# Performance work log

Hardware: AMD Instinct MI355X
Metric: run time of the kernel (lower is better)

Reference implementation:

```python
import jax, jax.numpy as jnp
import numpy as np

N_POINTS = 16384
N_SAMPLES = 8192


def setup_inputs() -> dict:
    key = jax.random.key(0)
    k1, k2, k3, k4 = jax.random.split(key, 4)
    a = jax.random.normal(k1, (3, N_POINTS), dtype=jnp.float32)
    b = jax.random.normal(k2, (3, N_POINTS), dtype=jnp.float32)
    # stand-ins for np.random.shuffle(...)[:n_samples] in the torch forward
    a_idx = jax.random.randint(k3, (N_SAMPLES,), 0, N_POINTS, dtype=jnp.int64)
    b_idx = jax.random.randint(k4, (N_SAMPLES,), 0, N_POINTS, dtype=jnp.int64)
    return {"a": a, "b": b, "a_idx": a_idx, "b_idx": b_idx}


def reference(a, b, a_idx, b_idx):
    # a, b: [3, N]; sample n_samples columns, transpose -> [n, 3], keep xyz
    pa = a[:, a_idx].T[:, :3]  # [n, 3]
    pb = b[:, b_idx].T[:, :3]  # [n, 3]
    # d[k, i] = ||pa_i - pb_k||^2, via ||a||^2 + ||b||^2 - 2 b.a^T
    # (avoids the original's [n, n, 3] broadcasted difference tensor)
    sq_a = jnp.sum(pa * pa, axis=1)  # [n]
    sq_b = jnp.sum(pb * pb, axis=1)  # [n]
    d = sq_a[None, :] + sq_b[:, None] - 2.0 * (pb @ pa.T)  # [n, n]
    # torch.min(d, 0)[0].sum(): min over b-points for each a-point, then sum
    return jnp.min(d, axis=0).sum()
```

## Files before the change

kernel.cpp:

```cpp
#include <hip/hip_runtime.h>
#include <stdint.h>


#define BLOCK   256
#define NPTS_A  8
#define BPTS    128

__device__ __forceinline__ unsigned enc_f32(float f) {
    unsigned u = __float_as_uint(f);
    return (u & 0x80000000u) ? ~u : (u | 0x80000000u);
}
__device__ __forceinline__ float dec_f32(unsigned u) {
    return (u & 0x80000000u) ? __uint_as_float(u & 0x7FFFFFFFu)
                             : __uint_as_float(~u);
}

__global__ __launch_bounds__(BLOCK)
void chamfer_min_kernel(const float* __restrict__ a,
                        const float* __restrict__ b,
                        const int* __restrict__ a_idx,
                        const int* __restrict__ b_idx,
                        unsigned* __restrict__ minarr,
                        int N, int a_chunks) {
    __shared__ float4 tile[BPTS];
    const int bid = blockIdx.x;
    const int ac  = bid % a_chunks;
    const int bc  = bid / a_chunks;
    const int tid = threadIdx.x;

    if (tid < BPTS) {
        int j  = bc * BPTS + tid;
        int bi = b_idx[j];
        float bx = b[bi], by = b[N + bi], bz = b[2 * N + bi];
        tile[tid] = make_float4(-2.f * bx, -2.f * by, -2.f * bz,
                                bx * bx + by * by + bz * bz);
    }
    __syncthreads();

    float ax[NPTS_A], ay[NPTS_A], az[NPTS_A], mn[NPTS_A];
    int   ii[NPTS_A];
#pragma unroll
    for (int m = 0; m < NPTS_A; ++m) {
        int i = ac * (BLOCK * NPTS_A) + m * BLOCK + tid;
        ii[m] = i;
        int ai = a_idx[i];
        ax[m] = a[ai]; ay[m] = a[N + ai]; az[m] = a[2 * N + ai];
        mn[m] = 3.4e38f;
    }

    for (int k = 0; k < BPTS; ++k) {
        float4 t = tile[k];
#pragma unroll
        for (int m = 0; m < NPTS_A; ++m) {
            float c = fmaf(t.x, ax[m], fmaf(t.y, ay[m], fmaf(t.z, az[m], t.w)));
            mn[m] = fminf(mn[m], c);
        }
    }

#pragma unroll
    for (int m = 0; m < NPTS_A; ++m)
        atomicMin(&minarr[ii[m]], enc_f32(mn[m]));
}

__global__ __launch_bounds__(BLOCK)
void chamfer_reduce_kernel(const float* __restrict__ a,
                           const int* __restrict__ a_idx,
                           const unsigned* __restrict__ minarr,
                           float* __restrict__ out, int N, int n) {
    int i = blockIdx.x * blockDim.x + threadIdx.x;
    float v = 0.f;
    if (i < n) {
        float f  = dec_f32(minarr[i]);
        int   ai = a_idx[i];
        float ax = a[ai], ay = a[N + ai], az = a[2 * N + ai];
        v = f + ax * ax + ay * ay + az * az;
    }
#pragma unroll
    for (int off = 32; off > 0; off >>= 1)
        v += __shfl_down(v, off, 64);
    if ((threadIdx.x & 63) == 0)
        atomicAdd(out, v);
}

extern "C" void kernel_launch(void* const* d_in, const int* in_sizes, int n_in,
                              void* d_out, int out_size, void* d_ws, size_t ws_size,
                              hipStream_t stream) {
    const float* a     = (const float*)d_in[0];
    const float* b     = (const float*)d_in[1];
    const int*   a_idx = (const int*)d_in[2];
    const int*   b_idx = (const int*)d_in[3];
    float*       out   = (float*)d_out;

    const int N = in_sizes[0] / 3;
    const int n = in_sizes[2];

    unsigned* minarr = (unsigned*)d_ws;

    hipMemsetAsync(minarr, 0xFF, (size_t)n * sizeof(unsigned), stream);
    hipMemsetAsync(out, 0, sizeof(float), stream);

    const int a_chunks = n / (BLOCK * NPTS_A);
    const int b_chunks = n / BPTS;
    chamfer_min_kernel<<<a_chunks * b_chunks, BLOCK, 0, stream>>>(
        a, b, a_idx, b_idx, minarr, N, a_chunks);

    chamfer_reduce_kernel<<<(n + BLOCK - 1) / BLOCK, BLOCK, 0, stream>>>(
        a, a_idx, minarr, out, N, n);
}
```

Baseline: 81.48 us.

## Replace atomicMin with per-chunk partial minima and deterministic two-stage reduction

```diff
diff --git a/kernel.cpp b/kernel.cpp
--- a/kernel.cpp
+++ b/kernel.cpp
@@ -4,24 +4,15 @@
 
 #define BLOCK   256
 #define NPTS_A  8
-#define BPTS    128
-
-__device__ __forceinline__ unsigned enc_f32(float f) {
-    unsigned u = __float_as_uint(f);
-    return (u & 0x80000000u) ? ~u : (u | 0x80000000u);
-}
-__device__ __forceinline__ float dec_f32(unsigned u) {
-    return (u & 0x80000000u) ? __uint_as_float(u & 0x7FFFFFFFu)
-                             : __uint_as_float(~u);
-}
+#define BPTS    64
 
 __global__ __launch_bounds__(BLOCK)
 void chamfer_min_kernel(const float* __restrict__ a,
                         const float* __restrict__ b,
                         const int* __restrict__ a_idx,
                         const int* __restrict__ b_idx,
-                        unsigned* __restrict__ minarr,
-                        int N, int a_chunks) {
+                        float* __restrict__ pmin,
+                        int N, int n, int a_chunks) {
     __shared__ float4 tile[BPTS];
     const int bid = blockIdx.x;
     const int ac  = bid % a_chunks;
@@ -38,16 +29,15 @@
     __syncthreads();
 
     float ax[NPTS_A], ay[NPTS_A], az[NPTS_A], mn[NPTS_A];
-    int   ii[NPTS_A];
 #pragma unroll
     for (int m = 0; m < NPTS_A; ++m) {
         int i = ac * (BLOCK * NPTS_A) + m * BLOCK + tid;
-        ii[m] = i;
         int ai = a_idx[i];
         ax[m] = a[ai]; ay[m] = a[N + ai]; az[m] = a[2 * N + ai];
         mn[m] = 3.4e38f;
     }
 
+#pragma unroll 4
     for (int k = 0; k < BPTS; ++k) {
         float4 t = tile[k];
 #pragma unroll
@@ -58,28 +48,52 @@
     }
 
 #pragma unroll
-    for (int m = 0; m < NPTS_A; ++m)
-        atomicMin(&minarr[ii[m]], enc_f32(mn[m]));
+    for (int m = 0; m < NPTS_A; ++m) {
+        int i = ac * (BLOCK * NPTS_A) + m * BLOCK + tid;
+        pmin[(size_t)bc * n + i] = mn[m];
+    }
 }
 
 __global__ __launch_bounds__(BLOCK)
-void chamfer_reduce_kernel(const float* __restrict__ a,
-                           const int* __restrict__ a_idx,
-                           const unsigned* __restrict__ minarr,
-                           float* __restrict__ out, int N, int n) {
-    int i = blockIdx.x * blockDim.x + threadIdx.x;
-    float v = 0.f;
-    if (i < n) {
-        float f  = dec_f32(minarr[i]);
-        int   ai = a_idx[i];
-        float ax = a[ai], ay = a[N + ai], az = a[2 * N + ai];
-        v = f + ax * ax + ay * ay + az * az;
-    }
+void chamfer_colmin_sum_kernel(const float* __restrict__ a,
+                               const int* __restrict__ a_idx,
+                               const float* __restrict__ pmin,
+                               float* __restrict__ psum,
+                               int N, int n, int b_chunks) {
+    __shared__ float wsum[BLOCK / 64];
+    const int tid = threadIdx.x;
+    const int i = blockIdx.x * BLOCK + tid;
+
+    float v = 3.4e38f;
+    for (int j = 0; j < b_chunks; ++j)
+        v = fminf(v, pmin[(size_t)j * n + i]);
+
+    int ai = a_idx[i];
+    float x = a[ai], y = a[N + ai], z = a[2 * N + ai];
+    v += x * x + y * y + z * z;
+
 #pragma unroll
     for (int off = 32; off > 0; off >>= 1)
         v += __shfl_down(v, off, 64);
-    if ((threadIdx.x & 63) == 0)
-        atomicAdd(out, v);
+    if ((tid & 63) == 0) wsum[tid >> 6] = v;
+    __syncthreads();
+    if (tid == 0) {
+        float s = 0.f;
+#pragma unroll
+        for (int w = 0; w < BLOCK / 64; ++w) s += wsum[w];
+        psum[blockIdx.x] = s;
+    }
+}
+
+__global__ __launch_bounds__(64)
+void chamfer_final_kernel(const float* __restrict__ psum,
+                          float* __restrict__ out, int nblocks) {
+    const int tid = threadIdx.x;
+    float v = (tid < nblocks) ? psum[tid] : 0.f;
+#pragma unroll
+    for (int off = 32; off > 0; off >>= 1)
+        v += __shfl_down(v, off, 64);
+    if (tid == 0) out[0] = v;
 }
 
 extern "C" void kernel_launch(void* const* d_in, const int* in_sizes, int n_in,
@@ -94,16 +108,18 @@
     const int N = in_sizes[0] / 3;
     const int n = in_sizes[2];
 
-    unsigned* minarr = (unsigned*)d_ws;
-
-    hipMemsetAsync(minarr, 0xFF, (size_t)n * sizeof(unsigned), stream);
-    hipMemsetAsync(out, 0, sizeof(float), stream);
-
     const int a_chunks = n / (BLOCK * NPTS_A);
     const int b_chunks = n / BPTS;
+    const int nblocks2 = n / BLOCK;
+
+    float* pmin = (float*)d_ws;
+    float* psum = pmin + (size_t)b_chunks * n;
+
     chamfer_min_kernel<<<a_chunks * b_chunks, BLOCK, 0, stream>>>(
-        a, b, a_idx, b_idx, minarr, N, a_chunks);
+        a, b, a_idx, b_idx, pmin, N, n, a_chunks);
 
-    chamfer_reduce_kernel<<<(n + BLOCK - 1) / BLOCK, BLOCK, 0, stream>>>(
-        a, a_idx, minarr, out, N, n);
+    chamfer_colmin_sum_kernel<<<nblocks2, BLOCK, 0, stream>>>(
+        a, a_idx, pmin, psum, N, n, b_chunks);
+
+    chamfer_final_kernel<<<1, 64, 0, stream>>>(psum, out, nblocks2);
 }
```

Measured after the change: 109.7 us. 1.35x slower.
